# Performance work log

Hardware: AMD Instinct MI355X
Metric: run time of the kernel (lower is better)

## Reference

```python
import jax, jax.numpy as jnp
import numpy as np

N_NODES = 50000
N_EDGES = 500000
IN_DIM = 256
HEADS = 4
OUT_C = 64
NEG_SLOPE = 0.2


def setup_inputs() -> dict:
    key = jax.random.key(0)
    ks = jax.random.split(key, 6)
    x = jax.random.normal(ks[0], (N_NODES, IN_DIM), dtype=jnp.float32)
    edge_index = jax.random.randint(ks[1], (2, N_EDGES), 0, N_NODES, dtype=jnp.int64)
    scale = 1.0 / np.sqrt(IN_DIM)
    W_l = jax.random.normal(ks[2], (IN_DIM, HEADS * OUT_C), dtype=jnp.float32) * scale
    W_r = jax.random.normal(ks[3], (IN_DIM, HEADS * OUT_C), dtype=jnp.float32) * scale
    b_l = jnp.zeros((HEADS * OUT_C,), dtype=jnp.float32)
    b_r = jnp.zeros((HEADS * OUT_C,), dtype=jnp.float32)
    att = jax.random.normal(ks[4], (HEADS, OUT_C), dtype=jnp.float32) * (1.0 / np.sqrt(OUT_C))
    bias = jnp.zeros((HEADS * OUT_C,), dtype=jnp.float32)
    return {"x": x, "edge_index": edge_index, "W_l": W_l, "b_l": b_l,
            "W_r": W_r, "b_r": b_r, "att": att, "bias": bias}


def _gatv2(x, edge_index, W_l, b_l, W_r, b_r, att, bias):
    N = x.shape[0]
    H, C = att.shape
    # add self loops (PyG GATv2Conv default add_self_loops=True)
    loop = jnp.arange(N, dtype=edge_index.dtype)
    src = jnp.concatenate([edge_index[0], loop])  # message sources (x_j)
    dst = jnp.concatenate([edge_index[1], loop])  # aggregation targets (x_i)
    x_l = (x @ W_l + b_l).reshape(N, H, C)  # source-side projection
    x_r = (x @ W_r + b_r).reshape(N, H, C)  # target-side projection
    # GATv2 attention logits: a^T LeakyReLU(x_l[src] + x_r[dst])
    e = jax.nn.leaky_relu(x_l[src] + x_r[dst], NEG_SLOPE)  # [E, H, C]
    logits = jnp.einsum('ehc,hc->eh', e, att)              # [E, H]
    # segmented softmax over incoming edges of each dst node
    m = jax.ops.segment_max(logits, dst, num_segments=N)   # [N, H]
    ex = jnp.exp(logits - m[dst])
    denom = jax.ops.segment_sum(ex, dst, num_segments=N)   # [N, H]
    alpha = ex / denom[dst]                                # [E, H]
    # weighted scatter-aggregation of source messages
    out = jax.ops.segment_sum(x_l[src] * alpha[:, :, None], dst, num_segments=N)  # [N, H, C]
    return out.reshape(N, H * C) + bias


def reference(x, edge_index, W_l, b_l, W_r, b_r, att, bias):
    out = _gatv2(x, edge_index, W_l, b_l, W_r, b_r, att, bias)  # [N, H*C]
    # wrapper: single relation -> reshape(-1, 1, output_dim) and cat on dim=1
    return out.reshape(-1, 1, HEADS * OUT_C)
```

## Files before the change

kernel.cpp:

```cpp
#include <hip/hip_runtime.h>
#include <hip/hip_bf16.h>
#include <math.h>

#define N_NODES 50000
#define N_PAD   50048
#define N_EDGES 500000
#define E_TOT   550000
#define HC      256
#define NHC     512
#define HEADS   4
#define NEG     0.2f

typedef __attribute__((ext_vector_type(8))) short short8;
typedef __attribute__((ext_vector_type(4))) float f32x4;
typedef __attribute__((ext_vector_type(2))) float f32x2;

__device__ __forceinline__ ushort f2bf(float f) {
    union { float f; unsigned u; } c; c.f = f;
    unsigned u = c.u;
    unsigned rounded = u + 0x7FFFu + ((u >> 16) & 1u);
    return (ushort)(rounded >> 16);
}

static constexpr size_t OFF_COUNTS = 0;
static constexpr size_t OFF_CUR    = OFF_COUNTS + (size_t)N_NODES * 4;
static constexpr size_t OFF_ROWS   = OFF_CUR + (size_t)N_NODES * 4;
static constexpr size_t OFF_SRCS   = OFF_ROWS + (size_t)(N_NODES + 1) * 4;
static constexpr size_t OFF_BSUM   = OFF_SRCS + (size_t)E_TOT * 4;
static constexpr size_t OFF_MODE   = OFF_BSUM + 64 * 4;
static constexpr size_t OFF_XB     = ((OFF_MODE + 4 + 255) / 256) * 256;
static constexpr size_t OFF_WT     = OFF_XB + (size_t)N_PAD * HC * 2;
static constexpr size_t OFF_XLB    = OFF_WT + (size_t)NHC * HC * 2;
static constexpr size_t OFF_XRB    = OFF_XLB + (size_t)N_NODES * HC * 2;

__device__ __forceinline__ int get_src(const int* __restrict__ ei, int mode, int e) {
    if (e >= N_EDGES) return e - N_EDGES;
    return mode ? ei[2 * e] : ei[e];
}
__device__ __forceinline__ int get_dst(const int* __restrict__ ei, int mode, int e) {
    if (e >= N_EDGES) return e - N_EDGES;
    return mode ? ei[2 * (N_EDGES + e)] : ei[N_EDGES + e];
}

#define XBLK 6256
#define WBLK 512
#define ZBLK 98
__global__ __launch_bounds__(256) void prep_kernel(
        const float* __restrict__ x, const float* __restrict__ Wl,
        const float* __restrict__ Wr, const int* __restrict__ ei,
        ushort* __restrict__ xb, ushort* __restrict__ wt,
        int* __restrict__ cz, int* __restrict__ mode) {
    const int b = blockIdx.x;
    if (b < XBLK) {
        size_t i = ((size_t)b * 256 + threadIdx.x) * 8;
        if (i >= (size_t)N_PAD * HC) return;
        ushort o[8];
        if (i < (size_t)N_NODES * HC) {
            float4 v0 = *(const float4*)(x + i);
            float4 v1 = *(const float4*)(x + i + 4);
            o[0] = f2bf(v0.x); o[1] = f2bf(v0.y); o[2] = f2bf(v0.z); o[3] = f2bf(v0.w);
            o[4] = f2bf(v1.x); o[5] = f2bf(v1.y); o[6] = f2bf(v1.z); o[7] = f2bf(v1.w);
        } else {
#pragma unroll
            for (int j = 0; j < 8; ++j) o[j] = 0;
        }
        *(short8*)(xb + i) = *(short8*)o;
    } else if (b < XBLK + WBLK) {
        int i = (b - XBLK) * 256 + threadIdx.x;
        int n = i >> 8, k = i & 255;
        float v = (n < HC) ? Wl[(size_t)k * HC + n] : Wr[(size_t)k * HC + (n - HC)];
        wt[i] = f2bf(v);
    } else if (b < XBLK + WBLK + ZBLK) {
        int i4 = (b - XBLK - WBLK) * 256 + threadIdx.x;
        if (i4 < 2 * N_NODES / 4) *(int4*)(cz + i4 * 4) = make_int4(0, 0, 0, 0);
    } else {
        __shared__ int any;
        if (threadIdx.x == 0) any = 0;
        __syncthreads();
        if (ei[2 * threadIdx.x + 1] != 0) atomicOr(&any, 1);
        __syncthreads();
        if (threadIdx.x == 0) mode[0] = (any == 0) ? 1 : 0;
    }
}

#define BM 128
#define BK 32
#define GEMM_BLKS 1564
#define CNT_BLKS  2149
__global__ __launch_bounds__(256) void gemm_count_kernel(
        const __hip_bfloat16* __restrict__ xb, const __hip_bfloat16* __restrict__ wt,
        const float* __restrict__ bl, const float* __restrict__ br,
        ushort* __restrict__ xlb, ushort* __restrict__ xrb,
        const int* __restrict__ ei, const int* __restrict__ mode,
        int* __restrict__ counts) {
    __shared__ ushort smem[4 * BM * BK];

    if (blockIdx.x >= GEMM_BLKS) {
        int e = (blockIdx.x - GEMM_BLKS) * 256 + threadIdx.x;
        if (e < E_TOT) atomicAdd(&counts[get_dst(ei, *mode, e)], 1);
        return;
    }

    auto AS = [&](int buf) { return (__hip_bfloat16*)(smem + buf * BM * BK); };
    auto BS = [&](int buf) { return (__hip_bfloat16*)(smem + 2 * BM * BK + buf * BM * BK); };
    const int t    = threadIdx.x;
    const int lane = t & 63;
    const int wid  = t >> 6;
    const int wr   = wid >> 1, wc = wid & 1;
    const int bx   = blockIdx.x % 391, by = blockIdx.x / 391;
    const int brow = bx * BM;
    const int bcol = by * BM;

    auto stage = [&](int buf, int k0) {
#pragma unroll
        for (int r = 0; r < 2; ++r) {
            int c = r * 256 + t;
            const __hip_bfloat16* ga = xb + ((size_t)(brow + (c >> 2)) * HC + k0 + (c & 3) * 8);
            __builtin_amdgcn_global_load_lds(
                (const __attribute__((address_space(1))) void*)ga,
                (__attribute__((address_space(3))) void*)((char*)AS(buf) + c * 16),
                16, 0, 0);
        }
#pragma unroll
        for (int r = 0; r < 2; ++r) {
            int c = r * 256 + t;
            const __hip_bfloat16* gb = wt + ((size_t)(bcol + (c >> 2)) * HC + k0 + (c & 3) * 8);
            __builtin_amdgcn_global_load_lds(
                (const __attribute__((address_space(1))) void*)gb,
                (__attribute__((address_space(3))) void*)((char*)BS(buf) + c * 16),
                16, 0, 0);
        }
    };

    f32x4 acc[4][4];
#pragma unroll
    for (int m = 0; m < 4; ++m)
#pragma unroll
        for (int n = 0; n < 4; ++n) acc[m][n] = (f32x4)0.f;

    stage(0, 0);
    __syncthreads();

    const int rsub = lane & 15;
    const int koff = (lane >> 4) * 16;

    for (int kk = 0; kk < 8; ++kk) {
        const int cur = kk & 1;
        if (kk < 7) stage(cur ^ 1, (kk + 1) * BK);
        short8 a[4], b[4];
#pragma unroll
        for (int m = 0; m < 4; ++m)
            a[m] = *(const short8*)((const char*)AS(cur) +
                    (wr * 64 + m * 16 + rsub) * (BK * 2) + koff);
#pragma unroll
        for (int n = 0; n < 4; ++n)
            b[n] = *(const short8*)((const char*)BS(cur) +
                    (wc * 64 + n * 16 + rsub) * (BK * 2) + koff);
#pragma unroll
        for (int m = 0; m < 4; ++m)
#pragma unroll
            for (int n = 0; n < 4; ++n)
                acc[m][n] = __builtin_amdgcn_mfma_f32_16x16x32_bf16(a[m], b[n], acc[m][n], 0, 0, 0);
        __syncthreads();
    }

    ushort* dst = (bcol < HC) ? xlb : xrb;
    const float* bvec = (bcol < HC) ? bl : br;
    const int cb = bcol & (HC - 1);
#pragma unroll
    for (int m = 0; m < 4; ++m) {
#pragma unroll
        for (int n = 0; n < 4; ++n) {
            int c_loc = wc * 64 + n * 16 + (lane & 15);
            float bv = bvec[cb + c_loc];
#pragma unroll
            for (int j = 0; j < 4; ++j) {
                int r_loc = wr * 64 + m * 16 + (lane >> 4) * 4 + j;
                smem[r_loc * 128 + (((c_loc >> 3) ^ (r_loc & 15)) * 8) + (c_loc & 7)] =
                    f2bf(acc[m][n][j] + bv);
            }
        }
    }
    __syncthreads();
    {
        const int r = t >> 1, hf = t & 1;
        if (brow + r < N_NODES) {
            ushort* gout = dst + (size_t)(brow + r) * HC + cb + hf * 64;
#pragma unroll
            for (int i = 0; i < 8; ++i) {
                int ci = hf * 8 + i;
                uint4 v = *(const uint4*)&smem[r * 128 + ((ci ^ (r & 15)) * 8)];
                *(uint4*)(gout + i * 8) = v;
            }
        }
    }
}

__global__ void scan1_kernel(const int* __restrict__ counts, int* __restrict__ rows,
                             int* __restrict__ bsum) {
    __shared__ int sdata[256];
    const int t = threadIdx.x;
    const int base = blockIdx.x * 1024 + t * 4;
    int v[4]; int s = 0;
#pragma unroll
    for (int j = 0; j < 4; ++j) {
        int idx = base + j;
        v[j] = (idx < N_NODES) ? counts[idx] : 0;
        s += v[j];
    }
    sdata[t] = s;
    __syncthreads();
    for (int off = 1; off < 256; off <<= 1) {
        int xv = (t >= off) ? sdata[t - off] : 0;
        __syncthreads();
        sdata[t] += xv;
        __syncthreads();
    }
    int run = sdata[t] - s;
#pragma unroll
    for (int j = 0; j < 4; ++j) {
        int idx = base + j;
        if (idx < N_NODES) rows[idx] = run;
        run += v[j];
    }
    if (t == 255) bsum[blockIdx.x] = sdata[255];
}

__global__ void scan3_kernel(int* __restrict__ rows, const int* __restrict__ bsum) {
    const int idx = blockIdx.x * 256 + threadIdx.x;
    const int r = blockIdx.x >> 2;
    const int lane = threadIdx.x & 63;
    int v = (lane < r) ? bsum[lane] : 0;
#pragma unroll
    for (int off = 1; off < 64; off <<= 1) v += __shfl_xor(v, off, 64);
    if (idx < N_NODES) rows[idx] += v;
    if (idx == 0) rows[N_NODES] = E_TOT;
}

__global__ void fill_kernel(const int* __restrict__ ei, const int* __restrict__ mode,
                            const int* __restrict__ rows, int* __restrict__ cursor,
                            int* __restrict__ srcs) {
    int e = blockIdx.x * blockDim.x + threadIdx.x;
    if (e < E_TOT) {
        int md = *mode;
        int d = get_dst(ei, md, e);
        int s = get_src(ei, md, e);
        int pos = atomicAdd(&cursor[d], 1);
        srcs[rows[d] + pos] = s;
    }
}

__global__ __launch_bounds__(256) void fused_agg_kernel(
        const ushort* __restrict__ xlb, const ushort* __restrict__ xrb,
        const float* __restrict__ att,
        const int* __restrict__ rows, const int* __restrict__ srcs,
        const float* __restrict__ bias, float* __restrict__ out) {
    const int lane = threadIdx.x & 63;
    const int n = (blockIdx.x * 256 + threadIdx.x) >> 6;
    if (n >= N_NODES) return;
    const int half = lane >> 5;
    const int sl   = lane & 31;
    const int start = rows[n], end = rows[n + 1];

    f32x2 xr2[4], at2[4];
    {
        uint4 c = *(const uint4*)(xrb + (size_t)n * HC + sl * 8);
        unsigned w[4] = {c.x, c.y, c.z, c.w};
#pragma unroll
        for (int j = 0; j < 4; ++j) {
            xr2[j][0] = __uint_as_float(w[j] << 16);
            xr2[j][1] = __uint_as_float(w[j] & 0xffff0000u);
        }
        float4 a0 = *(const float4*)&att[sl * 8];
        float4 a1 = *(const float4*)&att[sl * 8 + 4];
        at2[0][0] = a0.x; at2[0][1] = a0.y; at2[1][0] = a0.z; at2[1][1] = a0.w;
        at2[2][0] = a1.x; at2[2][1] = a1.y; at2[3][0] = a1.z; at2[3][1] = a1.w;
    }

    f32x2 acc2[4];
#pragma unroll
    for (int j = 0; j < 4; ++j) acc2[j] = (f32x2)0.f;
    float sm = 0.f;

    int i = start + half;
    uint4 rA = make_uint4(0, 0, 0, 0);
    int sB = -1;
    if (i < end) rA = *(const uint4*)(xlb + (size_t)srcs[i] * HC + sl * 8);
    if (i + 2 < end) sB = srcs[i + 2];

    for (; i < end; i += 2) {
        uint4 r = rA;
        if (sB >= 0) rA = *(const uint4*)(xlb + (size_t)sB * HC + sl * 8);
        sB = (i + 4 < end) ? srcs[i + 4] : -1;

        unsigned w[4] = {r.x, r.y, r.z, r.w};
        f32x2 xv[4];
#pragma unroll
        for (int j = 0; j < 4; ++j) {
            xv[j][0] = __uint_as_float(w[j] << 16);
            xv[j][1] = __uint_as_float(w[j] & 0xffff0000u);
        }

        f32x2 p2 = (f32x2)0.f;
#pragma unroll
        for (int j = 0; j < 4; ++j) {
            f32x2 v = xv[j] + xr2[j];
            f32x2 lk = __builtin_elementwise_max(v, v * NEG);
            p2 = lk * at2[j] + p2;
        }
        float p = p2[0] + p2[1];
        p += __shfl_xor(p, 1, 64);
        p += __shfl_xor(p, 2, 64);
        p += __shfl_xor(p, 4, 64);

        float wgt = __expf(p);
        sm += wgt;
        f32x2 w2; w2[0] = wgt; w2[1] = wgt;
#pragma unroll
        for (int j = 0; j < 4; ++j) acc2[j] = xv[j] * w2 + acc2[j];
    }

    sm += __shfl_xor(sm, 32, 64);
#pragma unroll
    for (int j = 0; j < 4; ++j) {
        acc2[j][0] += __shfl_xor(acc2[j][0], 32, 64);
        acc2[j][1] += __shfl_xor(acc2[j][1], 32, 64);
    }

    if (half == 0) {
        const float inv = 1.0f / sm;
        float4 b0 = *(const float4*)&bias[sl * 8];
        float4 b1 = *(const float4*)&bias[sl * 8 + 4];
        float4 o0, o1;
        o0.x = fmaf(acc2[0][0], inv, b0.x); o0.y = fmaf(acc2[0][1], inv, b0.y);
        o0.z = fmaf(acc2[1][0], inv, b0.z); o0.w = fmaf(acc2[1][1], inv, b0.w);
        o1.x = fmaf(acc2[2][0], inv, b1.x); o1.y = fmaf(acc2[2][1], inv, b1.y);
        o1.z = fmaf(acc2[3][0], inv, b1.z); o1.w = fmaf(acc2[3][1], inv, b1.w);
        *(float4*)&out[(size_t)n * HC + sl * 8]     = o0;
        *(float4*)&out[(size_t)n * HC + sl * 8 + 4] = o1;
    }
}

extern "C" void kernel_launch(void* const* d_in, const int* in_sizes, int n_in,
                              void* d_out, int out_size, void* d_ws, size_t ws_size,
                              hipStream_t stream) {
    const float* x    = (const float*)d_in[0];
    const int*   ei   = (const int*)d_in[1];
    const float* Wl   = (const float*)d_in[2];
    const float* bl   = (const float*)d_in[3];
    const float* Wr   = (const float*)d_in[4];
    const float* br   = (const float*)d_in[5];
    const float* att  = (const float*)d_in[6];
    const float* bias = (const float*)d_in[7];
    float* out = (float*)d_out;

    char* ws = (char*)d_ws;
    int*   counts = (int*)(ws + OFF_COUNTS);
    int*   cursor = (int*)(ws + OFF_CUR);
    int*   rows   = (int*)(ws + OFF_ROWS);
    int*   srcs   = (int*)(ws + OFF_SRCS);
    int*   bsum   = (int*)(ws + OFF_BSUM);
    int*   mode   = (int*)(ws + OFF_MODE);
    ushort* xb    = (ushort*)(ws + OFF_XB);
    ushort* wt    = (ushort*)(ws + OFF_WT);
    ushort* xlb   = (ushort*)(ws + OFF_XLB);
    ushort* xrb   = (ushort*)(ws + OFF_XRB);

    prep_kernel<<<XBLK + WBLK + ZBLK + 1, 256, 0, stream>>>(
        x, Wl, Wr, ei, xb, wt, counts, mode);

    gemm_count_kernel<<<GEMM_BLKS + CNT_BLKS, 256, 0, stream>>>(
        (const __hip_bfloat16*)xb, (const __hip_bfloat16*)wt, bl, br, xlb, xrb,
        ei, mode, counts);

    scan1_kernel<<<49, 256, 0, stream>>>(counts, rows, bsum);
    scan3_kernel<<<(N_NODES + 255) / 256, 256, 0, stream>>>(rows, bsum);

    fill_kernel<<<(E_TOT + 255) / 256, 256, 0, stream>>>(ei, mode, rows, cursor, srcs);

    fused_agg_kernel<<<(N_NODES + 3) / 4, 256, 0, stream>>>(
        xlb, xrb, att, rows, srcs, bias, out);
}
```

Measured before the change: 152.9 us.

## Single-buffer GEMM LDS, two-pass epilogue, and schedule count blocks first

The fused GEMM/count kernel drops the double-buffered LDS staging in favour of one buffer, halving shared memory from 32KB to 16KB so more blocks can fit per CU. The epilogue now writes the output tile in two column halves through the smaller buffer, adding extra barriers. The count (atomic histogram) blocks are moved to the front of the grid so they are dispatched before the GEMM blocks. The cost is that loads are no longer overlapped with MFMA inside a block, and latency hiding now depends on other resident blocks.

```diff
diff --git a/kernel.cpp b/kernel.cpp
--- a/kernel.cpp
+++ b/kernel.cpp
@@ -93,41 +93,42 @@
         ushort* __restrict__ xlb, ushort* __restrict__ xrb,
         const int* __restrict__ ei, const int* __restrict__ mode,
         int* __restrict__ counts) {
-    __shared__ ushort smem[4 * BM * BK];
-
-    if (blockIdx.x >= GEMM_BLKS) {
-        int e = (blockIdx.x - GEMM_BLKS) * 256 + threadIdx.x;
+    __shared__ ushort smem[2 * BM * BK];
+
+    if (blockIdx.x < CNT_BLKS) {
+        int e = blockIdx.x * 256 + threadIdx.x;
         if (e < E_TOT) atomicAdd(&counts[get_dst(ei, *mode, e)], 1);
         return;
     }
 
-    auto AS = [&](int buf) { return (__hip_bfloat16*)(smem + buf * BM * BK); };
-    auto BS = [&](int buf) { return (__hip_bfloat16*)(smem + 2 * BM * BK + buf * BM * BK); };
+    __hip_bfloat16* AS = (__hip_bfloat16*)smem;
+    __hip_bfloat16* BS = (__hip_bfloat16*)(smem + BM * BK);
     const int t    = threadIdx.x;
     const int lane = t & 63;
     const int wid  = t >> 6;
     const int wr   = wid >> 1, wc = wid & 1;
-    const int bx   = blockIdx.x % 391, by = blockIdx.x / 391;
+    const int gb   = blockIdx.x - CNT_BLKS;
+    const int bx   = gb % 391, by = gb / 391;
     const int brow = bx * BM;
     const int bcol = by * BM;
 
-    auto stage = [&](int buf, int k0) {
+    auto stage = [&](int k0) {
 #pragma unroll
         for (int r = 0; r < 2; ++r) {
             int c = r * 256 + t;
             const __hip_bfloat16* ga = xb + ((size_t)(brow + (c >> 2)) * HC + k0 + (c & 3) * 8);
             __builtin_amdgcn_global_load_lds(
                 (const __attribute__((address_space(1))) void*)ga,
-                (__attribute__((address_space(3))) void*)((char*)AS(buf) + c * 16),
+                (__attribute__((address_space(3))) void*)((char*)AS + c * 16),
                 16, 0, 0);
         }
 #pragma unroll
         for (int r = 0; r < 2; ++r) {
             int c = r * 256 + t;
-            const __hip_bfloat16* gb = wt + ((size_t)(bcol + (c >> 2)) * HC + k0 + (c & 3) * 8);
+            const __hip_bfloat16* gb2 = wt + ((size_t)(bcol + (c >> 2)) * HC + k0 + (c & 3) * 8);
             __builtin_amdgcn_global_load_lds(
-                (const __attribute__((address_space(1))) void*)gb,
-                (__attribute__((address_space(3))) void*)((char*)BS(buf) + c * 16),
+                (const __attribute__((address_space(1))) void*)gb2,
+                (__attribute__((address_space(3))) void*)((char*)BS + c * 16),
                 16, 0, 0);
         }
     };
@@ -137,24 +138,21 @@
     for (int m = 0; m < 4; ++m)
 #pragma unroll
         for (int n = 0; n < 4; ++n) acc[m][n] = (f32x4)0.f;
-
-    stage(0, 0);
-    __syncthreads();
 
     const int rsub = lane & 15;
     const int koff = (lane >> 4) * 16;
 
     for (int kk = 0; kk < 8; ++kk) {
-        const int cur = kk & 1;
-        if (kk < 7) stage(cur ^ 1, (kk + 1) * BK);
+        stage(kk * BK);
+        __syncthreads();
         short8 a[4], b[4];
 #pragma unroll
         for (int m = 0; m < 4; ++m)
-            a[m] = *(const short8*)((const char*)AS(cur) +
+            a[m] = *(const short8*)((const char*)AS +
                     (wr * 64 + m * 16 + rsub) * (BK * 2) + koff);
 #pragma unroll
         for (int n = 0; n < 4; ++n)
-            b[n] = *(const short8*)((const char*)BS(cur) +
+            b[n] = *(const short8*)((const char*)BS +
                     (wc * 64 + n * 16 + rsub) * (BK * 2) + koff);
 #pragma unroll
         for (int m = 0; m < 4; ++m)
@@ -168,31 +166,37 @@
     const float* bvec = (bcol < HC) ? bl : br;
     const int cb = bcol & (HC - 1);
 #pragma unroll
-    for (int m = 0; m < 4; ++m) {
-#pragma unroll
-        for (int n = 0; n < 4; ++n) {
-            int c_loc = wc * 64 + n * 16 + (lane & 15);
-            float bv = bvec[cb + c_loc];
-#pragma unroll
-            for (int j = 0; j < 4; ++j) {
-                int r_loc = wr * 64 + m * 16 + (lane >> 4) * 4 + j;
-                smem[r_loc * 128 + (((c_loc >> 3) ^ (r_loc & 15)) * 8) + (c_loc & 7)] =
-                    f2bf(acc[m][n][j] + bv);
+    for (int p = 0; p < 2; ++p) {
+        if (wc == p) {
+#pragma unroll
+            for (int m = 0; m < 4; ++m) {
+#pragma unroll
+                for (int n = 0; n < 4; ++n) {
+                    int c_h = n * 16 + rsub;
+                    float bv = bvec[cb + p * 64 + c_h];
+#pragma unroll
+                    for (int j = 0; j < 4; ++j) {
+                        int r_loc = wr * 64 + m * 16 + (lane >> 4) * 4 + j;
+                        smem[r_loc * 64 + (((c_h >> 3) ^ (r_loc & 7)) * 8) + (c_h & 7)] =
+                            f2bf(acc[m][n][j] + bv);
+                    }
+                }
             }
         }
-    }
-    __syncthreads();
-    {
-        const int r = t >> 1, hf = t & 1;
-        if (brow + r < N_NODES) {
-            ushort* gout = dst + (size_t)(brow + r) * HC + cb + hf * 64;
-#pragma unroll
-            for (int i = 0; i < 8; ++i) {
-                int ci = hf * 8 + i;
-                uint4 v = *(const uint4*)&smem[r * 128 + ((ci ^ (r & 15)) * 8)];
-                *(uint4*)(gout + i * 8) = v;
+        __syncthreads();
+        {
+            const int r = t >> 1, sub = t & 1;
+            if (brow + r < N_NODES) {
+                ushort* gout = dst + (size_t)(brow + r) * HC + cb + p * 64 + sub * 32;
+#pragma unroll
+                for (int i = 0; i < 4; ++i) {
+                    int ci = sub * 4 + i;
+                    uint4 v = *(const uint4*)&smem[r * 64 + ((ci ^ (r & 7)) * 8)];
+                    *(uint4*)(gout + i * 8) = v;
+                }
             }
         }
+        __syncthreads();
     }
 }
 
@@ -369,7 +373,7 @@
     prep_kernel<<<XBLK + WBLK + ZBLK + 1, 256, 0, stream>>>(
         x, Wl, Wr, ei, xb, wt, counts, mode);
 
-    gemm_count_kernel<<<GEMM_BLKS + CNT_BLKS, 256, 0, stream>>>(
+    gemm_count_kernel<<<CNT_BLKS + GEMM_BLKS, 256, 0, stream>>>(
         (const __hip_bfloat16*)xb, (const __hip_bfloat16*)wt, bl, br, xlb, xrb,
         ei, mode, counts);
 
```

Measured after the change: 162.8 us. 1.06x slower.
